# Optimization experiments

Hardware: AMD Instinct MI355X
Metric: run time of the kernel (lower is better)

## Reference

```python
import jax, jax.numpy as jnp
import numpy as np
import math

N_PTS = 131072
K_GAUSS = 2048


def quat_to_rotmat(q):
    # q: (K,4) -> (K,3,3), normalized unit quaternion to rotation matrix
    q = q / jnp.linalg.norm(q, axis=-1, keepdims=True)
    w, x, y, z = q[:, 0], q[:, 1], q[:, 2], q[:, 3]
    R = jnp.stack([
        jnp.stack([1 - 2 * (y * y + z * z), 2 * (x * y - w * z), 2 * (x * z + w * y)], axis=-1),
        jnp.stack([2 * (x * y + w * z), 1 - 2 * (x * x + z * z), 2 * (y * z - w * x)], axis=-1),
        jnp.stack([2 * (x * z - w * y), 2 * (y * z + w * x), 1 - 2 * (x * x + y * y)], axis=-1),
    ], axis=-2)
    return R


def setup_inputs() -> dict:
    key = jax.random.key(0)
    k1, k2, k3, k4 = jax.random.split(key, 4)
    x = jax.random.normal(k1, (N_PTS, 3), dtype=jnp.float32) * 0.5
    means = jax.random.normal(k2, (K_GAUSS, 3), dtype=jnp.float32) * 0.1
    log_scales = jnp.full((K_GAUSS, 3), math.log(0.05), dtype=jnp.float32)
    # identity-ish quaternions with small perturbation (as after some training)
    q = jnp.concatenate([jnp.ones((K_GAUSS, 1), jnp.float32),
                         0.1 * jax.random.normal(k3, (K_GAUSS, 3), dtype=jnp.float32)], axis=-1)
    log_amplitudes = jnp.full((K_GAUSS,), math.log(0.1), dtype=jnp.float32) \
        + 0.1 * jax.random.normal(k4, (K_GAUSS,), dtype=jnp.float32)
    return {"x": x, "means": means, "log_scales": log_scales,
            "quaternions": q, "log_amplitudes": log_amplitudes}


def reference(x, means, log_scales, quaternions, log_amplitudes):
    # amplitudes
    amps = jnp.exp(jnp.clip(log_amplitudes, -10.0, 6.0))            # (K,)
    # covariance Sigma = R diag(s^2) R^T, regularized
    s = jnp.clip(jnp.exp(log_scales), 1e-5, 100.0)                  # (K,3)
    R = quat_to_rotmat(quaternions)                                 # (K,3,3)
    Sigma = jnp.einsum('kij,kj,klj->kil', R, s * s, R)              # (K,3,3)
    Sigma_reg = Sigma + 1e-5 * jnp.eye(3, dtype=Sigma.dtype)
    # Mahalanobis via precision A = Sigma_reg^{-1} (math-equivalent to the
    # Cholesky triangular solve in the original: mahal = diff^T A diff)
    A = jnp.linalg.inv(Sigma_reg)                                   # (K,3,3), SPD
    b = jnp.einsum('kij,kj->ki', A, means)                          # (K,3)
    c = jnp.einsum('ki,ki->k', b, means)                            # (K,)
    # mahal[n,k] = x_n^T A_k x_n - 2 x_n . b_k + c_k  (no (N,K,3) diff tensor)
    xx = x[:, :, None] * x[:, None, :]                              # (N,3,3)
    mahal = jnp.einsum('nij,kij->nk', xx, A) - 2.0 * (x @ b.T) + c[None, :]
    # weighted sum over Gaussians
    out = jnp.exp(-0.5 * mahal) @ amps                              # (N,)
    return out
```

## Files before the change

kernel.cpp:

```cpp
#include <hip/hip_runtime.h>
#include <math.h>


typedef _Float16 half8 __attribute__((ext_vector_type(8)));
typedef float    f32x4 __attribute__((ext_vector_type(4)));

#define WPB     4
#define CHUNK   8
#define NBUF    2

#define EXP_SCALE 8388608.0f
#define EXP_BIAS  1064880938.0f

__device__ __forceinline__ unsigned cvt_u32_sat(float y) {
    unsigned u;
    asm("v_cvt_u32_f32 %0, %1" : "=v"(u) : "v"(y));
    return u;
}

__global__ __launch_bounds__(256) void gmf_precompute(
        const float* __restrict__ means,
        const float* __restrict__ log_scales,
        const float* __restrict__ quats,
        const float* __restrict__ log_amps,
        _Float16* __restrict__ Bf, int K, int KT) {
    int k = blockIdx.x * blockDim.x + threadIdx.x;
    if (k >= KT * 16) return;

    float gc[10];
    if (k < K) {
        float qw = quats[4*k+0], qx = quats[4*k+1], qy = quats[4*k+2], qz = quats[4*k+3];
        float qn = rsqrtf(qw*qw + qx*qx + qy*qy + qz*qz);
        qw *= qn; qx *= qn; qy *= qn; qz *= qn;

        float r00 = 1.f - 2.f*(qy*qy + qz*qz);
        float r01 = 2.f*(qx*qy - qw*qz);
        float r02 = 2.f*(qx*qz + qw*qy);
        float r10 = 2.f*(qx*qy + qw*qz);
        float r11 = 1.f - 2.f*(qx*qx + qz*qz);
        float r12 = 2.f*(qy*qz - qw*qx);
        float r20 = 2.f*(qx*qz - qw*qy);
        float r21 = 2.f*(qy*qz + qw*qx);
        float r22 = 1.f - 2.f*(qx*qx + qy*qy);

        float s0 = fminf(fmaxf(expf(log_scales[3*k+0]), 1e-5f), 100.f);
        float s1 = fminf(fmaxf(expf(log_scales[3*k+1]), 1e-5f), 100.f);
        float s2 = fminf(fmaxf(expf(log_scales[3*k+2]), 1e-5f), 100.f);
        float v0 = s0*s0, v1 = s1*s1, v2 = s2*s2;

        float S00 = r00*r00*v0 + r01*r01*v1 + r02*r02*v2 + 1e-5f;
        float S11 = r10*r10*v0 + r11*r11*v1 + r12*r12*v2 + 1e-5f;
        float S22 = r20*r20*v0 + r21*r21*v1 + r22*r22*v2 + 1e-5f;
        float S01 = r00*r10*v0 + r01*r11*v1 + r02*r12*v2;
        float S02 = r00*r20*v0 + r01*r21*v1 + r02*r22*v2;
        float S12 = r10*r20*v0 + r11*r21*v1 + r12*r22*v2;

        float c00 = S11*S22 - S12*S12;
        float c01 = S02*S12 - S01*S22;
        float c02 = S01*S12 - S02*S11;
        float det = S00*c00 + S01*c01 + S02*c02;
        float id  = 1.f/det;
        float A00 = c00*id, A01 = c01*id, A02 = c02*id;
        float A11 = (S00*S22 - S02*S02)*id;
        float A12 = (S01*S02 - S00*S12)*id;
        float A22 = (S00*S11 - S01*S01)*id;

        float m0 = means[3*k+0], m1 = means[3*k+1], m2 = means[3*k+2];
        float b0 = A00*m0 + A01*m1 + A02*m2;
        float b1 = A01*m0 + A11*m1 + A12*m2;
        float b2 = A02*m0 + A12*m1 + A22*m2;
        float cc = b0*m0 + b1*m1 + b2*m2;

        float la = fminf(fmaxf(log_amps[k], -10.f), 6.f);
        const float L2E = 1.4426950408889634f;
        const float h = -0.5f * L2E;

        gc[0] = h*A00; gc[1] = h*A11; gc[2] = h*A22;
        gc[3] = 2.f*h*A01; gc[4] = 2.f*h*A02; gc[5] = 2.f*h*A12;
        gc[6] = L2E*b0; gc[7] = L2E*b1; gc[8] = L2E*b2;
        gc[9] = h*cc + L2E*la;
    } else {
        #pragma unroll
        for (int j = 0; j < 10; ++j) gc[j] = 0.f;
        gc[9] = -60000.f;
    }

    _Float16 gh[10], gl[10];
    #pragma unroll
    for (int j = 0; j < 10; ++j) {
        gh[j] = (_Float16)gc[j];
        gl[j] = (_Float16)(gc[j] - (float)gh[j]);
    }

    int kt = k >> 4, c = k & 15;
    _Float16* dst = Bf + (size_t)kt * 64 * 8;
    #pragma unroll 32
    for (int r = 0; r < 32; ++r) {
        int lg = r >> 3, j = r & 7;
        _Float16 v = (r < 10) ? gh[r]
                   : (r < 20) ? gl[r-10]
                   : (r < 30) ? gh[r-20]
                   : (_Float16)0.f;
        dst[((size_t)lg*16 + c)*8 + j] = v;
    }
}

__device__ __forceinline__ half8 gmf_build_afr1(
        const float* __restrict__ x, int pt, int lane, int N, int PTtot) {
    int lr = lane & 15;
    int lg = lane >> 4;
    int n = pt * 16 + lr;
    float x0 = 0.f, x1 = 0.f, x2 = 0.f;
    if (pt < PTtot && n < N) { x0 = x[3*n]; x1 = x[3*n+1]; x2 = x[3*n+2]; }

    float P0 = x0*x0, P1 = x1*x1, P2 = x2*x2;
    float P3 = x0*x1, P4 = x0*x2, P5 = x1*x2;

    _Float16 h0 = (_Float16)P0, h1 = (_Float16)P1, h2 = (_Float16)P2;
    _Float16 h3 = (_Float16)P3, h4 = (_Float16)P4, h5 = (_Float16)P5;
    _Float16 h6 = (_Float16)x0, h7 = (_Float16)x1, h8 = (_Float16)x2;
    _Float16 h9 = (_Float16)1.f;
    _Float16 l0 = (_Float16)(P0 - (float)h0), l1 = (_Float16)(P1 - (float)h1);
    _Float16 l2 = (_Float16)(P2 - (float)h2), l3 = (_Float16)(P3 - (float)h3);
    _Float16 l4 = (_Float16)(P4 - (float)h4), l5 = (_Float16)(P5 - (float)h5);
    _Float16 l6 = (_Float16)(x0 - (float)h6), l7 = (_Float16)(x1 - (float)h7);
    _Float16 l8 = (_Float16)(x2 - (float)h8), l9 = (_Float16)0.f;
    _Float16 z  = (_Float16)0.f;

    half8 a;
    if      (lg == 0) a = (half8){h0,h1,h2,h3,h4,h5,h6,h7};
    else if (lg == 1) a = (half8){h8,h9,h0,h1,h2,h3,h4,h5};
    else if (lg == 2) a = (half8){h6,h7,h8,h9,l0,l1,l2,l3};
    else              a = (half8){l4,l5,l6,l7,l8,l9,z,z};
    return a;
}

#define GMF_EXPACC(CC)                                                          \
    {                                                                           \
        f32x4 y = __builtin_elementwise_fma((CC), vscale, vbias);               \
        acc.x += __uint_as_float(cvt_u32_sat(y.x));                             \
        acc.y += __uint_as_float(cvt_u32_sat(y.y));                             \
        acc.z += __uint_as_float(cvt_u32_sat(y.z));                             \
        acc.w += __uint_as_float(cvt_u32_sat(y.w));                             \
    }

__global__ __launch_bounds__(256, 8) void gmf_main_ns(
        const float* __restrict__ x,
        const _Float16* __restrict__ Bfh,
        float* __restrict__ out,
        int N, int KT, int PTtot) {
    __shared__ _Float16 lbs_raw[NBUF * CHUNK * 512];

    int tid  = threadIdx.x;
    int lane = tid & 63;
    int wid  = tid >> 6;
    int pt   = blockIdx.x * WPB + wid;
    bool active = pt < PTtot;

    half8 afr = gmf_build_afr1(x, pt, lane, N, PTtot);
    f32x4 acc = {0.f, 0.f, 0.f, 0.f};
    const f32x4 czero  = {0.f, 0.f, 0.f, 0.f};
    const f32x4 vscale = {EXP_SCALE, EXP_SCALE, EXP_SCALE, EXP_SCALE};
    const f32x4 vbias  = {EXP_BIAS,  EXP_BIAS,  EXP_BIAS,  EXP_BIAS};

    int nchunks = (KT + CHUNK - 1) / CHUNK;

#define GMF_STAGE(BUF, KBASE, NK)                                               \
    {                                                                           \
        _Pragma("unroll")                                                       \
        for (int j = 0; j < 2; ++j) {                                           \
            int tile = wid * 2 + j;                                             \
            if (tile < (NK)) {                                \
                const _Float16* src = Bfh + ((size_t)((KBASE) + tile)) * 512    \
                                          + lane * 8;                           \
                __builtin_amdgcn_global_load_lds(                               \
                    (const __attribute__((address_space(1))) void*)src,         \
                    (__attribute__((address_space(3))) void*)                   \
                        (lbs_raw + ((BUF) * CHUNK + tile) * 512 + lane * 8),    \
                    16, 0, 0);                                                  \
            }                                                                   \
        }                                                                       \
    }

    {
        int nk0 = min(CHUNK, KT);
        GMF_STAGE(0, 0, nk0)
    }
    __syncthreads();

    for (int c = 0; c < nchunks; ++c) {
        int cb = c & 1;
        int kbase = c * CHUNK;
        int nk = min(CHUNK, KT - kbase);

        if (c + 1 < nchunks) {
            int nk1 = min(CHUNK, KT - (c + 1) * CHUNK);
            GMF_STAGE(cb ^ 1, (c + 1) * CHUNK, nk1)
        }

        if (active) {
            const half8* cur = (const half8*)(lbs_raw + cb * CHUNK * 512);
            if (nk == CHUNK) {
                f32x4 cc[CHUNK];
                #pragma unroll
                for (int i = 0; i < CHUNK; ++i) {
                    half8 b = cur[i * 64 + lane];
                    cc[i] = __builtin_amdgcn_mfma_f32_16x16x32_f16(
                        afr, b, czero, 0, 0, 0);
                    if (i >= 2) GMF_EXPACC(cc[i - 2])
                }
                GMF_EXPACC(cc[CHUNK - 2])
                GMF_EXPACC(cc[CHUNK - 1])
            } else {
                for (int i = 0; i < nk; ++i) {
                    half8 b = cur[i * 64 + lane];
                    f32x4 cc = __builtin_amdgcn_mfma_f32_16x16x32_f16(
                        afr, b, czero, 0, 0, 0);
                    GMF_EXPACC(cc)
                }
            }
        }

        __syncthreads();
    }

    if (active) {
        int lr = lane & 15;
        int lg = lane >> 4;
        f32x4 a = acc;
        #pragma unroll
        for (int m = 1; m <= 8; m <<= 1) {
            a.x += __shfl_xor(a.x, m);
            a.y += __shfl_xor(a.y, m);
            a.z += __shfl_xor(a.z, m);
            a.w += __shfl_xor(a.w, m);
        }
        if (lr == 0) {
            int n0 = pt * 16 + lg * 4;
            if (n0     < N) out[n0]     = a.x;
            if (n0 + 1 < N) out[n0 + 1] = a.y;
            if (n0 + 2 < N) out[n0 + 2] = a.z;
            if (n0 + 3 < N) out[n0 + 3] = a.w;
        }
    }
#undef GMF_STAGE
}

extern "C" void kernel_launch(void* const* d_in, const int* in_sizes, int n_in,
                              void* d_out, int out_size, void* d_ws, size_t ws_size,
                              hipStream_t stream) {
    const float* x          = (const float*)d_in[0];
    const float* means      = (const float*)d_in[1];
    const float* log_scales = (const float*)d_in[2];
    const float* quats      = (const float*)d_in[3];
    const float* log_amps   = (const float*)d_in[4];
    float* out = (float*)d_out;

    int K = in_sizes[4];
    int N = out_size;
    int KT = (K + 15) / 16;
    int PTtot = (N + 15) / 16;

    _Float16* Bf = (_Float16*)d_ws;

    gmf_precompute<<<(KT*16 + 255) / 256, 256, 0, stream>>>(
        means, log_scales, quats, log_amps, Bf, K, KT);

    int blocks = (PTtot + WPB - 1) / WPB;
    gmf_main_ns<<<blocks, 256, 0, stream>>>(x, Bf, out, N, KT, PTtot);
}
```

Before: 42.19 us.

## Process two point tiles per wave to reuse each loaded Gaussian B fragment

Each wave now handles two 16-point tiles, building two A fragments and issuing two MFMAs per LDS-loaded B fragment, with separate accumulators. This halves the LDS reads and the global-to-LDS staging work per point, and halves the block count. The cost is more registers per wave and fewer blocks, which may reduce occupancy or leave the GPU underfilled. The exp/accumulate work per point is unchanged.

```diff
diff --git a/kernel.cpp b/kernel.cpp
--- a/kernel.cpp
+++ b/kernel.cpp
@@ -6,6 +6,7 @@
 typedef float    f32x4 __attribute__((ext_vector_type(4)));
 
 #define WPB     4
+#define PT      2
 #define CHUNK   8
 #define NBUF    2
 
@@ -135,14 +136,34 @@
     return a;
 }
 
-#define GMF_EXPACC(CC)                                                          \
+#define GMF_EXPACC(CC, ACC)                                                     \
     {                                                                           \
         f32x4 y = __builtin_elementwise_fma((CC), vscale, vbias);               \
-        acc.x += __uint_as_float(cvt_u32_sat(y.x));                             \
-        acc.y += __uint_as_float(cvt_u32_sat(y.y));                             \
-        acc.z += __uint_as_float(cvt_u32_sat(y.z));                             \
-        acc.w += __uint_as_float(cvt_u32_sat(y.w));                             \
-    }
+        (ACC).x += __uint_as_float(cvt_u32_sat(y.x));                           \
+        (ACC).y += __uint_as_float(cvt_u32_sat(y.y));                           \
+        (ACC).z += __uint_as_float(cvt_u32_sat(y.z));                           \
+        (ACC).w += __uint_as_float(cvt_u32_sat(y.w));                           \
+    }
+
+__device__ __forceinline__ void gmf_epilogue1(
+        f32x4 a, int pt, int lane, int N, int PTtot, float* __restrict__ out) {
+    int lr = lane & 15;
+    int lg = lane >> 4;
+    #pragma unroll
+    for (int m = 1; m <= 8; m <<= 1) {
+        a.x += __shfl_xor(a.x, m);
+        a.y += __shfl_xor(a.y, m);
+        a.z += __shfl_xor(a.z, m);
+        a.w += __shfl_xor(a.w, m);
+    }
+    if (lr == 0 && pt < PTtot) {
+        int n0 = pt * 16 + lg * 4;
+        if (n0     < N) out[n0]     = a.x;
+        if (n0 + 1 < N) out[n0 + 1] = a.y;
+        if (n0 + 2 < N) out[n0 + 2] = a.z;
+        if (n0 + 3 < N) out[n0 + 3] = a.w;
+    }
+}
 
 __global__ __launch_bounds__(256, 8) void gmf_main_ns(
         const float* __restrict__ x,
@@ -154,11 +175,14 @@
     int tid  = threadIdx.x;
     int lane = tid & 63;
     int wid  = tid >> 6;
-    int pt   = blockIdx.x * WPB + wid;
-    bool active = pt < PTtot;
-
-    half8 afr = gmf_build_afr1(x, pt, lane, N, PTtot);
-    f32x4 acc = {0.f, 0.f, 0.f, 0.f};
+    int pt0  = (blockIdx.x * WPB + wid) * PT;
+    int pt1  = pt0 + 1;
+    bool active = pt0 < PTtot;
+
+    half8 afr0 = gmf_build_afr1(x, pt0, lane, N, PTtot);
+    half8 afr1 = gmf_build_afr1(x, pt1, lane, N, PTtot);
+    f32x4 acc0 = {0.f, 0.f, 0.f, 0.f};
+    f32x4 acc1 = {0.f, 0.f, 0.f, 0.f};
     const f32x4 czero  = {0.f, 0.f, 0.f, 0.f};
     const f32x4 vscale = {EXP_SCALE, EXP_SCALE, EXP_SCALE, EXP_SCALE};
     const f32x4 vbias  = {EXP_BIAS,  EXP_BIAS,  EXP_BIAS,  EXP_BIAS};
@@ -201,22 +225,32 @@
         if (active) {
             const half8* cur = (const half8*)(lbs_raw + cb * CHUNK * 512);
             if (nk == CHUNK) {
-                f32x4 cc[CHUNK];
+                half8 b = cur[lane];
+                f32x4 cB0 = __builtin_amdgcn_mfma_f32_16x16x32_f16(afr0, b, czero, 0, 0, 0);
+                f32x4 cB1 = __builtin_amdgcn_mfma_f32_16x16x32_f16(afr1, b, czero, 0, 0, 0);
+                b = cur[64 + lane];
+                f32x4 cA0 = __builtin_amdgcn_mfma_f32_16x16x32_f16(afr0, b, czero, 0, 0, 0);
+                f32x4 cA1 = __builtin_amdgcn_mfma_f32_16x16x32_f16(afr1, b, czero, 0, 0, 0);
                 #pragma unroll
-                for (int i = 0; i < CHUNK; ++i) {
-                    half8 b = cur[i * 64 + lane];
-                    cc[i] = __builtin_amdgcn_mfma_f32_16x16x32_f16(
-                        afr, b, czero, 0, 0, 0);
-                    if (i >= 2) GMF_EXPACC(cc[i - 2])
+                for (int i = 2; i < CHUNK; ++i) {
+                    GMF_EXPACC(cB0, acc0)
+                    GMF_EXPACC(cB1, acc1)
+                    cB0 = cA0; cB1 = cA1;
+                    b = cur[i * 64 + lane];
+                    cA0 = __builtin_amdgcn_mfma_f32_16x16x32_f16(afr0, b, czero, 0, 0, 0);
+                    cA1 = __builtin_amdgcn_mfma_f32_16x16x32_f16(afr1, b, czero, 0, 0, 0);
                 }
-                GMF_EXPACC(cc[CHUNK - 2])
-                GMF_EXPACC(cc[CHUNK - 1])
+                GMF_EXPACC(cB0, acc0)
+                GMF_EXPACC(cB1, acc1)
+                GMF_EXPACC(cA0, acc0)
+                GMF_EXPACC(cA1, acc1)
             } else {
                 for (int i = 0; i < nk; ++i) {
                     half8 b = cur[i * 64 + lane];
-                    f32x4 cc = __builtin_amdgcn_mfma_f32_16x16x32_f16(
-                        afr, b, czero, 0, 0, 0);
-                    GMF_EXPACC(cc)
+                    f32x4 c0 = __builtin_amdgcn_mfma_f32_16x16x32_f16(afr0, b, czero, 0, 0, 0);
+                    f32x4 c1 = __builtin_amdgcn_mfma_f32_16x16x32_f16(afr1, b, czero, 0, 0, 0);
+                    GMF_EXPACC(c0, acc0)
+                    GMF_EXPACC(c1, acc1)
                 }
             }
         }
@@ -225,23 +259,8 @@
     }
 
     if (active) {
-        int lr = lane & 15;
-        int lg = lane >> 4;
-        f32x4 a = acc;
-        #pragma unroll
-        for (int m = 1; m <= 8; m <<= 1) {
-            a.x += __shfl_xor(a.x, m);
-            a.y += __shfl_xor(a.y, m);
-            a.z += __shfl_xor(a.z, m);
-            a.w += __shfl_xor(a.w, m);
-        }
-        if (lr == 0) {
-            int n0 = pt * 16 + lg * 4;
-            if (n0     < N) out[n0]     = a.x;
-            if (n0 + 1 < N) out[n0 + 1] = a.y;
-            if (n0 + 2 < N) out[n0 + 2] = a.z;
-            if (n0 + 3 < N) out[n0 + 3] = a.w;
-        }
+        gmf_epilogue1(acc0, pt0, lane, N, PTtot, out);
+        gmf_epilogue1(acc1, pt1, lane, N, PTtot, out);
     }
 #undef GMF_STAGE
 }
@@ -266,6 +285,7 @@
     gmf_precompute<<<(KT*16 + 255) / 256, 256, 0, stream>>>(
         means, log_scales, quats, log_amps, Bf, K, KT);
 
-    int blocks = (PTtot + WPB - 1) / WPB;
+    int tiles_per_block = WPB * PT;
+    int blocks = (PTtot + tiles_per_block - 1) / tiles_per_block;
     gmf_main_ns<<<blocks, 256, 0, stream>>>(x, Bf, out, N, KT, PTtot);
 }
```

Measured after the change: 103.3 us. 2.45x slower.
